# Kernel optimization log

Measured on AMD Instinct MI355X. Metric: run time of the kernel, lower is better.

Reference implementation:

```python
import jax, jax.numpy as jnp
import numpy as np

EPS = 1e-5


def instance_norm(x):
    # InstanceNorm2d(affine=False): normalize each (b, c) map over spatial dims
    mean = x.mean(axis=(2, 3), keepdims=True)
    var = ((x - mean) ** 2).mean(axis=(2, 3), keepdims=True)
    return (x - mean) / jnp.sqrt(var + EPS)


def adder_conv_transpose(x, w, stride, padding):
    """AdderNet transposed 'convolution': standard transposed-conv geometry
    (zero-dilate input by stride, pad by k-1-padding, slide flipped kernel),
    but with the multiply-accumulate replaced by negative L1 distance:
        out[b,co,h,w] = -sum_{ci,i,j} |x_patch[b,ci,h+i,w+j] - w_flip[co,ci,i,j]|
    x: (B, Cin, H, W); w: (Cin, Cout, k, k) as in nn.ConvTranspose2d.
    """
    Cin, Cout, k, _ = w.shape
    B, _, H, W = x.shape
    s = stride
    Hd, Wd = (H - 1) * s + 1, (W - 1) * s + 1
    xd = jnp.zeros((B, Cin, Hd, Wd), x.dtype).at[:, :, ::s, ::s].set(x)
    p = k - 1 - padding
    xp = jnp.pad(xd, ((0, 0), (0, 0), (p, p), (p, p)))
    wf = jnp.flip(w, axis=(2, 3)).transpose(1, 0, 2, 3)  # (Cout, Cin, k, k)
    Ho = Hd + 2 * p - k + 1
    Wo = Wd + 2 * p - k + 1
    out = jnp.zeros((B, Cout, Ho, Wo), x.dtype)
    # fixed k*k taps (<=16): accumulate -|patch - weight| summed over Cin
    for i in range(k):
        for j in range(k):
            patch = xp[:, :, i:i + Ho, j:j + Wo]  # (B, Cin, Ho, Wo)
            wij = wf[:, :, i, j][None, :, :, None, None]  # (1, Cout, Cin, 1, 1)
            out = out - jnp.abs(patch[:, None] - wij).sum(axis=2)
    return out


_CFG = [  # (Cin, Cout, k, stride, pad)
    (100, 128, 4, 2, 1),
    (128, 64, 4, 2, 1),
    (64, 32, 3, 2, 1),
    (32, 16, 4, 2, 1),
    (16, 1, 4, 2, 1),
]


def setup_inputs() -> dict:
    key = jax.random.key(0)
    ks = jax.random.split(key, 6)
    inp = {"x": jax.random.normal(ks[0], (512, 100, 1, 1), dtype=jnp.float32)}
    for li, (cin, cout, k, _, _) in enumerate(_CFG):
        inp[f"w{li + 1}"] = 0.1 * jax.random.normal(ks[li + 1], (cin, cout, k, k), dtype=jnp.float32)
    return inp


def reference(x, w1, w2, w3, w4, w5):
    h = x
    for w, (_, _, k, s, p) in zip((w1, w2, w3, w4, w5), _CFG):
        h = adder_conv_transpose(h, w, s, p)
        h = instance_norm(h)
        h = jax.nn.relu(h)
    # final activation is Tanh (last ReLU in loop replaced below)
    return jnp.tanh(instance_norm(adder_conv_transpose_final_fixup(h)))


# NOTE: structure above would double-apply the last layer; define reference cleanly instead.

def adder_conv_transpose_final_fixup(h):  # placeholder, unused
    return h


def reference(x, w1, w2, w3, w4, w5):  # noqa: F811 (clean final definition)
    ws = (w1, w2, w3, w4, w5)
    h = x
    for li, (w, (_, _, k, s, p)) in enumerate(zip(ws, _CFG)):
        h = instance_norm(adder_conv_transpose(h, w, s, p))
        h = jnp.tanh(h) if li == 4 else jax.nn.relu(h)
    return h  # (B, 1, 28, 28)
```

## Files before the change

### kernel.cpp

```cpp
#include <hip/hip_runtime.h>
#include <math.h>


#define OFF_T1 0
#define OFF_T2 2048
#define OFF_T3 3072
#define OFF_T4 3360
#define OFF_T5 3616
#define OFF_S  3632
#define OFF_WT1 4096
#define OFF_WT2 208896
#define OFF_WT3 339968
#define OFF_WT4 358400
#define OFF_WT5 366592
#define OFF_BUF0 366848
#define OFF_BUF1 1169664

__global__ __launch_bounds__(256) void prep1(const float* __restrict__ w1, const float* __restrict__ w2,
                      const float* __restrict__ w3, const float* __restrict__ w4,
                      const float* __restrict__ w5, float* __restrict__ ws) {
  int idx = blockIdx.x * 256 + threadIdx.x;
  if (idx < 362752) {
    const float* W; int CIN, COUT, KK, e, wtb;
    if (idx < 204800)      { W=w1; CIN=100; COUT=128; KK=16; e=idx;        wtb=OFF_WT1; }
    else if (idx < 335872) { W=w2; CIN=128; COUT=64;  KK=16; e=idx-204800; wtb=OFF_WT2; }
    else if (idx < 354304) { W=w3; CIN=64;  COUT=32;  KK=9;  e=idx-335872; wtb=OFF_WT3; }
    else if (idx < 362496) { W=w4; CIN=32;  COUT=16;  KK=16; e=idx-354304; wtb=OFF_WT4; }
    else                   { W=w5; CIN=16;  COUT=1;   KK=16; e=idx-362496; wtb=OFF_WT5; }
    int ci = e / (COUT*KK); int rem = e % (COUT*KK); int co = rem / KK; int r = rem % KK;
    ws[wtb + ((r*(CIN/4) + (ci>>2))*COUT + co)*4 + (ci&3)] = W[e];
  }
  if (idx < 3632) {
    const float* W; int CIN, COUT, KK, local;
    if (idx < 2048)      { W=w1; CIN=100; COUT=128; KK=16; local=idx; }
    else if (idx < 3072) { W=w2; CIN=128; COUT=64;  KK=16; local=idx-2048; }
    else if (idx < 3360) { W=w3; CIN=64;  COUT=32;  KK=9;  local=idx-3072; }
    else if (idx < 3616) { W=w4; CIN=32;  COUT=16;  KK=16; local=idx-3360; }
    else                 { W=w5; CIN=16;  COUT=1;   KK=16; local=idx-3616; }
    int co = local / KK, r = local % KK;
    float s = 0.f;
    for (int ci = 0; ci < CIN; ++ci) s += fabsf(W[(ci*COUT + co)*KK + r]);
    ws[idx] = s;
  }
}

__global__ __launch_bounds__(256) void prep2(float* __restrict__ ws) {
  int idx = threadIdx.x;
  if (idx >= 241) return;
  int tb, KK;
  if (idx < 128)      { tb = OFF_T1 + idx*16;       KK=16; }
  else if (idx < 192) { tb = OFF_T2 + (idx-128)*16; KK=16; }
  else if (idx < 224) { tb = OFF_T3 + (idx-192)*9;  KK=9;  }
  else if (idx < 240) { tb = OFF_T4 + (idx-224)*16; KK=16; }
  else                { tb = OFF_T5;                KK=16; }
  float s = 0.f;
  for (int r = 0; r < KK; ++r) s += ws[tb + r];
  ws[OFF_S + idx] = s;
}

template<int CIN, int COUT, int K, int STRIDE, int PAD,
         int HI, int WI, int HO, int WO, int ACT, int CP>
__global__ __launch_bounds__(256)
void layer_kernel(const float* __restrict__ X, const float* __restrict__ WT,
                  const float* __restrict__ T, const float* __restrict__ SS,
                  float* __restrict__ Y) {
  constexpr int S = HO*WO;
  constexpr int HIWI = HI*WI;
  constexpr int NIN = CIN*HIWI;
  constexpr int CIN4 = CIN/4;
  __shared__ float xst[HIWI*CIN];
  __shared__ float outs[S*CP];
  __shared__ float stat_mean[COUT], stat_rstd[COUT];
  __shared__ float wred[8];
  const int b = blockIdx.x;
  const int tid = threadIdx.x;

  for (int i = tid; i < NIN; i += 256) {
    int ci = i / HIWI, p = i % HIWI;
    xst[p*CIN + ci] = X[b*NIN + i];
  }
  __syncthreads();

  for (int idx = tid; idx < COUT*S; idx += 256) {
    const int co = idx % COUT;
    const int s  = idx / COUT;
    const int oh = s / WO, ow = s % WO;
    float acc = SS[co];
    #pragma unroll
    for (int kh = 0; kh < K; ++kh) {
      const int th = oh + PAD - kh;
      if (th < 0) continue;
      if (th % STRIDE) continue;
      const int ih = th / STRIDE;
      if (ih >= HI) continue;
      #pragma unroll
      for (int kw = 0; kw < K; ++kw) {
        const int tw = ow + PAD - kw;
        if (tw < 0) continue;
        if (tw % STRIDE) continue;
        const int iw = tw / STRIDE;
        if (iw >= WI) continue;
        const int r = kh*K + kw;
        acc -= T[co*(K*K) + r];
        const float4* xp4 = reinterpret_cast<const float4*>(&xst[(ih*WI + iw)*CIN]);
        const float4* wp4 = reinterpret_cast<const float4*>(WT) + (size_t)r*CIN4*COUT + co;
        float a0=0.f, a1=0.f, a2=0.f, a3=0.f;
        #pragma unroll 2
        for (int c4 = 0; c4 < CIN4; ++c4) {
          float4 xv = xp4[c4];
          float4 wv = wp4[(size_t)c4*COUT];
          a0 += fabsf(xv.x - wv.x);
          a1 += fabsf(xv.y - wv.y);
          a2 += fabsf(xv.z - wv.z);
          a3 += fabsf(xv.w - wv.w);
        }
        acc += (a0+a1) + (a2+a3);
      }
    }
    outs[s*CP + co] = -acc;
  }
  __syncthreads();

  if constexpr (COUT == 1) {
    float p = 0.f;
    for (int s2 = tid; s2 < S; s2 += 256) p += outs[s2];
    #pragma unroll
    for (int off = 1; off < 64; off <<= 1) p += __shfl_xor(p, off, 64);
    if ((tid & 63) == 0) wred[tid >> 6] = p;
    __syncthreads();
    const float mean = (wred[0]+wred[1]+wred[2]+wred[3]) * (1.f/S);
    float q = 0.f;
    for (int s2 = tid; s2 < S; s2 += 256) { float d = outs[s2]-mean; q += d*d; }
    #pragma unroll
    for (int off = 1; off < 64; off <<= 1) q += __shfl_xor(q, off, 64);
    __syncthreads();
    if ((tid & 63) == 0) wred[tid >> 6] = q;
    __syncthreads();
    const float rstd = rsqrtf((wred[0]+wred[1]+wred[2]+wred[3]) * (1.f/S) + 1e-5f);
    if (tid == 0) { stat_mean[0] = mean; stat_rstd[0] = rstd; }
    __syncthreads();
  } else {
    constexpr int G = 256 / COUT;
    const int g = tid / G;
    const int j = tid % G;
    float p = 0.f;
    for (int s2 = j; s2 < S; s2 += G) p += outs[s2*CP + g];
    #pragma unroll
    for (int off = 1; off < G; off <<= 1) p += __shfl_xor(p, off, 64);
    const float mean = p * (1.f/S);
    float q = 0.f;
    for (int s2 = j; s2 < S; s2 += G) { float d = outs[s2*CP + g] - mean; q += d*d; }
    #pragma unroll
    for (int off = 1; off < G; off <<= 1) q += __shfl_xor(q, off, 64);
    const float rstd = rsqrtf(q * (1.f/S) + 1e-5f);
    if (j == 0) { stat_mean[g] = mean; stat_rstd[g] = rstd; }
    __syncthreads();
  }

  for (int idx = tid; idx < COUT*S; idx += 256) {
    const int co = idx / S;
    const int s2 = idx % S;
    float v = (outs[s2*CP + co] - stat_mean[co]) * stat_rstd[co];
    v = ACT ? tanhf(v) : fmaxf(v, 0.f);
    Y[(size_t)b*(COUT*S) + idx] = v;
  }
}

extern "C" void kernel_launch(void* const* d_in, const int* in_sizes, int n_in,
                              void* d_out, int out_size, void* d_ws, size_t ws_size,
                              hipStream_t stream) {
  const float* x  = (const float*)d_in[0];
  const float* w1 = (const float*)d_in[1];
  const float* w2 = (const float*)d_in[2];
  const float* w3 = (const float*)d_in[3];
  const float* w4 = (const float*)d_in[4];
  const float* w5 = (const float*)d_in[5];
  float* ws  = (float*)d_ws;
  float* out = (float*)d_out;

  prep1<<<1417, 256, 0, stream>>>(w1, w2, w3, w4, w5, ws);
  prep2<<<1, 256, 0, stream>>>(ws);

  float* A1 = ws + OFF_BUF0;
  float* A2 = ws + OFF_BUF1;
  float* A3 = ws + OFF_BUF0;
  float* A4 = ws + OFF_BUF1;

  layer_kernel<100, 128, 4, 2, 1,  1, 1,  2, 2,  0, 129><<<512,256,0,stream>>>(x,  ws+OFF_WT1, ws+OFF_T1, ws+OFF_S,       A1);
  layer_kernel<128,  64, 4, 2, 1,  2, 2,  4, 4,  0,  65><<<512,256,0,stream>>>(A1, ws+OFF_WT2, ws+OFF_T2, ws+OFF_S+128,   A2);
  layer_kernel< 64,  32, 3, 2, 1,  4, 4,  7, 7,  0,  33><<<512,256,0,stream>>>(A2, ws+OFF_WT3, ws+OFF_T3, ws+OFF_S+192,   A3);
  layer_kernel< 32,  16, 4, 2, 1,  7, 7, 14,14,  0,  17><<<512,256,0,stream>>>(A3, ws+OFF_WT4, ws+OFF_T4, ws+OFF_S+224,   A4);
  layer_kernel< 16,   1, 4, 2, 1, 14,14, 28,28,  1,   1><<<512,256,0,stream>>>(A4, ws+OFF_WT5, ws+OFF_T5, ws+OFF_S+240,   out);
}
```

Before: 304.5 us.

## Restructure layers into batch-parallel conv kernels plus separate norm kernels

Replaces the per-sample fused layer kernel with a conv kernel that puts the batch on lanes (activations stored channel-major with batch innermost), register-tiles over output channels and batch, and splits the Cin reduction across blocks for some layers. Instance norm, ReLU and tanh move into separate norm kernels that also sum the Cin partial results. Padding taps are folded in through precomputed per-tap weight abs sums. The aim is better weight reuse across the batch and more parallelism, at the cost of extra launches and global round trips for the intermediate results.

Result: faster. 253.8 us (-16.7%).

```diff
diff --git a/kernel.cpp b/kernel.cpp
--- a/kernel.cpp
+++ b/kernel.cpp
@@ -1,24 +1,33 @@
 #include <hip/hip_runtime.h>
 #include <math.h>
 
+#define NB 512
 
 #define OFF_T1 0
 #define OFF_T2 2048
 #define OFF_T3 3072
 #define OFF_T4 3360
 #define OFF_T5 3616
-#define OFF_S  3632
 #define OFF_WT1 4096
 #define OFF_WT2 208896
 #define OFF_WT3 339968
 #define OFF_WT4 358400
 #define OFF_WT5 366592
-#define OFF_BUF0 366848
-#define OFF_BUF1 1169664
-
-__global__ __launch_bounds__(256) void prep1(const float* __restrict__ w1, const float* __restrict__ w2,
-                      const float* __restrict__ w3, const float* __restrict__ w4,
-                      const float* __restrict__ w5, float* __restrict__ ws) {
+#define OFF_ACT 366848
+#define OFF_Y   1972480
+
+__device__ __forceinline__ void loadv(float (&d)[1], const float* p){ d[0]=*p; }
+__device__ __forceinline__ void loadv(float (&d)[2], const float* p){ float2 v=*reinterpret_cast<const float2*>(p); d[0]=v.x; d[1]=v.y; }
+__device__ __forceinline__ void loadv(float (&d)[4], const float* p){ float4 v=*reinterpret_cast<const float4*>(p); d[0]=v.x; d[1]=v.y; d[2]=v.z; d[3]=v.w; }
+__device__ __forceinline__ void storev(float* p, const float (&d)[1]){ *p=d[0]; }
+__device__ __forceinline__ void storev(float* p, const float (&d)[2]){ *reinterpret_cast<float2*>(p)=make_float2(d[0],d[1]); }
+__device__ __forceinline__ void storev(float* p, const float (&d)[4]){ *reinterpret_cast<float4*>(p)=make_float4(d[0],d[1],d[2],d[3]); }
+
+__global__ __launch_bounds__(256)
+void prep1(const float* __restrict__ w1, const float* __restrict__ w2,
+           const float* __restrict__ w3, const float* __restrict__ w4,
+           const float* __restrict__ w5, const float* __restrict__ x,
+           float* __restrict__ ws) {
   int idx = blockIdx.x * 256 + threadIdx.x;
   if (idx < 362752) {
     const float* W; int CIN, COUT, KK, e, wtb;
@@ -28,141 +37,185 @@
     else if (idx < 362496) { W=w4; CIN=32;  COUT=16;  KK=16; e=idx-354304; wtb=OFF_WT4; }
     else                   { W=w5; CIN=16;  COUT=1;   KK=16; e=idx-362496; wtb=OFF_WT5; }
     int ci = e / (COUT*KK); int rem = e % (COUT*KK); int co = rem / KK; int r = rem % KK;
-    ws[wtb + ((r*(CIN/4) + (ci>>2))*COUT + co)*4 + (ci&3)] = W[e];
-  }
-  if (idx < 3632) {
-    const float* W; int CIN, COUT, KK, local;
-    if (idx < 2048)      { W=w1; CIN=100; COUT=128; KK=16; local=idx; }
-    else if (idx < 3072) { W=w2; CIN=128; COUT=64;  KK=16; local=idx-2048; }
-    else if (idx < 3360) { W=w3; CIN=64;  COUT=32;  KK=9;  local=idx-3072; }
-    else if (idx < 3616) { W=w4; CIN=32;  COUT=16;  KK=16; local=idx-3360; }
-    else                 { W=w5; CIN=16;  COUT=1;   KK=16; local=idx-3616; }
-    int co = local / KK, r = local % KK;
-    float s = 0.f;
-    for (int ci = 0; ci < CIN; ++ci) s += fabsf(W[(ci*COUT + co)*KK + r]);
-    ws[idx] = s;
-  }
-}
-
-__global__ __launch_bounds__(256) void prep2(float* __restrict__ ws) {
-  int idx = threadIdx.x;
-  if (idx >= 241) return;
-  int tb, KK;
-  if (idx < 128)      { tb = OFF_T1 + idx*16;       KK=16; }
-  else if (idx < 192) { tb = OFF_T2 + (idx-128)*16; KK=16; }
-  else if (idx < 224) { tb = OFF_T3 + (idx-192)*9;  KK=9;  }
-  else if (idx < 240) { tb = OFF_T4 + (idx-224)*16; KK=16; }
-  else                { tb = OFF_T5;                KK=16; }
+    ws[wtb + (r*CIN + ci)*COUT + co] = W[e];
+  } else {
+    int j = idx - 362752;
+    int b = j / 100, ci = j % 100;
+    ws[OFF_ACT + ci*NB + b] = x[j];
+  }
+}
+
+__global__ __launch_bounds__(256)
+void prep2(float* __restrict__ ws) {
+  int t = blockIdx.x * 256 + threadIdx.x;
+  if (t >= 3632) return;
+  int CIN, COUT, wtb, tb, local;
+  if (t < 2048)      { CIN=100; COUT=128; wtb=OFF_WT1; tb=OFF_T1; local=t; }
+  else if (t < 3072) { CIN=128; COUT=64;  wtb=OFF_WT2; tb=OFF_T2; local=t-2048; }
+  else if (t < 3360) { CIN=64;  COUT=32;  wtb=OFF_WT3; tb=OFF_T3; local=t-3072; }
+  else if (t < 3616) { CIN=32;  COUT=16;  wtb=OFF_WT4; tb=OFF_T4; local=t-3360; }
+  else               { CIN=16;  COUT=1;   wtb=OFF_WT5; tb=OFF_T5; local=t-3616; }
+  int r = local / COUT, co = local % COUT;
+  const float* wp = ws + wtb + (r*CIN)*COUT + co;
   float s = 0.f;
-  for (int r = 0; r < KK; ++r) s += ws[tb + r];
-  ws[OFF_S + idx] = s;
-}
-
-template<int CIN, int COUT, int K, int STRIDE, int PAD,
-         int HI, int WI, int HO, int WO, int ACT, int CP>
-__global__ __launch_bounds__(256)
-void layer_kernel(const float* __restrict__ X, const float* __restrict__ WT,
-                  const float* __restrict__ T, const float* __restrict__ SS,
-                  float* __restrict__ Y) {
-  constexpr int S = HO*WO;
-  constexpr int HIWI = HI*WI;
-  constexpr int NIN = CIN*HIWI;
-  constexpr int CIN4 = CIN/4;
-  __shared__ float xst[HIWI*CIN];
-  __shared__ float outs[S*CP];
-  __shared__ float stat_mean[COUT], stat_rstd[COUT];
-  __shared__ float wred[8];
-  const int b = blockIdx.x;
-  const int tid = threadIdx.x;
-
-  for (int i = tid; i < NIN; i += 256) {
-    int ci = i / HIWI, p = i % HIWI;
-    xst[p*CIN + ci] = X[b*NIN + i];
-  }
-  __syncthreads();
-
-  for (int idx = tid; idx < COUT*S; idx += 256) {
-    const int co = idx % COUT;
-    const int s  = idx / COUT;
-    const int oh = s / WO, ow = s % WO;
-    float acc = SS[co];
+  for (int ci = 0; ci < CIN; ++ci) s += fabsf(wp[ci*COUT]);
+  ws[tb + local] = s;
+}
+
+template<int CIN,int COUT,int K,int PAD,int HI,int WI,int HO,int WO,int R_CO,int R_B,int CS>
+__global__ __launch_bounds__(64)
+void conv_kernel(const float* __restrict__ X, const float* __restrict__ W,
+                 const float* __restrict__ T, float* __restrict__ Y) {
+  constexpr int S = HO*WO, NCOG = COUT/R_CO, NBG = NB/(64*R_B), CINS = CIN/CS;
+  const int wid = blockIdx.x;
+  const int q   = wid % S;
+  const int t1  = wid / S;
+  const int cog = t1 % NCOG;
+  const int t2  = t1 / NCOG;
+  const int bg  = t2 % NBG;
+  const int cs  = t2 / NBG;
+  const int oh = q / WO, ow = q % WO;
+  const int co0 = cog * R_CO;
+  const int b0  = bg*(64*R_B) + (int)threadIdx.x * R_B;
+  const int ci0 = cs * CINS;
+
+  float acc[R_CO][R_B];
+  #pragma unroll
+  for (int rc = 0; rc < R_CO; ++rc)
+    #pragma unroll
+    for (int rb = 0; rb < R_B; ++rb) acc[rc][rb] = 0.f;
+
+  if (cs == 0) {
+    float init[R_CO];
+    #pragma unroll
+    for (int rc = 0; rc < R_CO; ++rc) init[rc] = 0.f;
     #pragma unroll
     for (int kh = 0; kh < K; ++kh) {
-      const int th = oh + PAD - kh;
-      if (th < 0) continue;
-      if (th % STRIDE) continue;
-      const int ih = th / STRIDE;
-      if (ih >= HI) continue;
       #pragma unroll
       for (int kw = 0; kw < K; ++kw) {
-        const int tw = ow + PAD - kw;
-        if (tw < 0) continue;
-        if (tw % STRIDE) continue;
-        const int iw = tw / STRIDE;
-        if (iw >= WI) continue;
-        const int r = kh*K + kw;
-        acc -= T[co*(K*K) + r];
-        const float4* xp4 = reinterpret_cast<const float4*>(&xst[(ih*WI + iw)*CIN]);
-        const float4* wp4 = reinterpret_cast<const float4*>(WT) + (size_t)r*CIN4*COUT + co;
-        float a0=0.f, a1=0.f, a2=0.f, a3=0.f;
-        #pragma unroll 2
-        for (int c4 = 0; c4 < CIN4; ++c4) {
-          float4 xv = xp4[c4];
-          float4 wv = wp4[(size_t)c4*COUT];
-          a0 += fabsf(xv.x - wv.x);
-          a1 += fabsf(xv.y - wv.y);
-          a2 += fabsf(xv.z - wv.z);
-          a3 += fabsf(xv.w - wv.w);
+        const int th = oh + PAD - kh, tw = ow + PAD - kw;
+        const bool real = (th >= 0) && !(th & 1) && ((th >> 1) < HI)
+                       && (tw >= 0) && !(tw & 1) && ((tw >> 1) < WI);
+        if (!real) {
+          const float* tp = T + (kh*K + kw)*COUT + co0;
+          #pragma unroll
+          for (int rc = 0; rc < R_CO; ++rc) init[rc] += tp[rc];
         }
-        acc += (a0+a1) + (a2+a3);
       }
     }
-    outs[s*CP + co] = -acc;
-  }
-  __syncthreads();
-
-  if constexpr (COUT == 1) {
-    float p = 0.f;
-    for (int s2 = tid; s2 < S; s2 += 256) p += outs[s2];
-    #pragma unroll
-    for (int off = 1; off < 64; off <<= 1) p += __shfl_xor(p, off, 64);
-    if ((tid & 63) == 0) wred[tid >> 6] = p;
-    __syncthreads();
-    const float mean = (wred[0]+wred[1]+wred[2]+wred[3]) * (1.f/S);
-    float q = 0.f;
-    for (int s2 = tid; s2 < S; s2 += 256) { float d = outs[s2]-mean; q += d*d; }
-    #pragma unroll
-    for (int off = 1; off < 64; off <<= 1) q += __shfl_xor(q, off, 64);
-    __syncthreads();
-    if ((tid & 63) == 0) wred[tid >> 6] = q;
-    __syncthreads();
-    const float rstd = rsqrtf((wred[0]+wred[1]+wred[2]+wred[3]) * (1.f/S) + 1e-5f);
-    if (tid == 0) { stat_mean[0] = mean; stat_rstd[0] = rstd; }
-    __syncthreads();
-  } else {
-    constexpr int G = 256 / COUT;
-    const int g = tid / G;
-    const int j = tid % G;
-    float p = 0.f;
-    for (int s2 = j; s2 < S; s2 += G) p += outs[s2*CP + g];
-    #pragma unroll
-    for (int off = 1; off < G; off <<= 1) p += __shfl_xor(p, off, 64);
-    const float mean = p * (1.f/S);
-    float q = 0.f;
-    for (int s2 = j; s2 < S; s2 += G) { float d = outs[s2*CP + g] - mean; q += d*d; }
-    #pragma unroll
-    for (int off = 1; off < G; off <<= 1) q += __shfl_xor(q, off, 64);
-    const float rstd = rsqrtf(q * (1.f/S) + 1e-5f);
-    if (j == 0) { stat_mean[g] = mean; stat_rstd[g] = rstd; }
-    __syncthreads();
-  }
-
-  for (int idx = tid; idx < COUT*S; idx += 256) {
-    const int co = idx / S;
-    const int s2 = idx % S;
-    float v = (outs[s2*CP + co] - stat_mean[co]) * stat_rstd[co];
-    v = ACT ? tanhf(v) : fmaxf(v, 0.f);
-    Y[(size_t)b*(COUT*S) + idx] = v;
+    #pragma unroll
+    for (int rc = 0; rc < R_CO; ++rc)
+      #pragma unroll
+      for (int rb = 0; rb < R_B; ++rb) acc[rc][rb] = init[rc];
+  }
+
+  #pragma unroll
+  for (int kh = 0; kh < K; ++kh) {
+    const int th = oh + PAD - kh;
+    if (th < 0 || (th & 1)) continue;
+    const int ih = th >> 1;
+    if (ih >= HI) continue;
+    #pragma unroll
+    for (int kw = 0; kw < K; ++kw) {
+      const int tw = ow + PAD - kw;
+      if (tw < 0 || (tw & 1)) continue;
+      const int iw = tw >> 1;
+      if (iw >= WI) continue;
+      const int r = kh*K + kw, p = ih*WI + iw;
+      const float* xp = X + (p*CIN + ci0)*NB + b0;
+      const float* wp = W + (r*CIN + ci0)*COUT + co0;
+      #pragma unroll 4
+      for (int ci = 0; ci < CINS; ++ci) {
+        float xv[R_B];
+        loadv(xv, xp + ci*NB);
+        #pragma unroll
+        for (int rc = 0; rc < R_CO; ++rc) {
+          const float wv = wp[ci*COUT + rc];
+          #pragma unroll
+          for (int rb = 0; rb < R_B; ++rb)
+            acc[rc][rb] += fabsf(xv[rb] - wv);
+        }
+      }
+    }
+  }
+
+  float* yp = Y + ((cs*S + q)*COUT + co0)*NB + b0;
+  #pragma unroll
+  for (int rc = 0; rc < R_CO; ++rc) storev(yp + rc*NB, acc[rc]);
+}
+
+template<int COUT,int S,int CS>
+__global__ __launch_bounds__(256)
+void norm_kernel(const float* __restrict__ Y, float* __restrict__ A) {
+  __shared__ float red[4][64];
+  __shared__ float stat[2][64];
+  const int co = blockIdx.x % COUT;
+  const int bg = blockIdx.x / COUT;
+  const int lane = threadIdx.x & 63;
+  const int w = threadIdx.x >> 6;
+  const int b = bg*64 + lane;
+  const float* yb = Y + co*NB + b;
+
+  float s = 0.f;
+  for (int q = w; q < S; q += 4) {
+    float v = 0.f;
+    #pragma unroll
+    for (int cs = 0; cs < CS; ++cs) v += yb[(cs*S + q)*COUT*NB];
+    s += v;
+  }
+  red[w][lane] = s;
+  __syncthreads();
+  if (w == 0) stat[0][lane] = (red[0][lane]+red[1][lane]+red[2][lane]+red[3][lane]) * (1.f/S);
+  __syncthreads();
+  const float mu = stat[0][lane];
+
+  float s2 = 0.f;
+  for (int q = w; q < S; q += 4) {
+    float v = 0.f;
+    #pragma unroll
+    for (int cs = 0; cs < CS; ++cs) v += yb[(cs*S + q)*COUT*NB];
+    const float d = v - mu;
+    s2 += d*d;
+  }
+  red[w][lane] = s2;
+  __syncthreads();
+  if (w == 0) stat[1][lane] = rsqrtf((red[0][lane]+red[1][lane]+red[2][lane]+red[3][lane]) * (1.f/S) + 1e-5f);
+  __syncthreads();
+  const float rs = stat[1][lane];
+
+  for (int q = w; q < S; q += 4) {
+    float v = 0.f;
+    #pragma unroll
+    for (int cs = 0; cs < CS; ++cs) v += yb[(cs*S + q)*COUT*NB];
+    const float n = (mu - v) * rs;
+    A[(q*COUT + co)*NB + b] = fmaxf(n, 0.f);
+  }
+}
+
+__global__ __launch_bounds__(256)
+void norm5_kernel(const float* __restrict__ Y, float* __restrict__ out) {
+  const int w = threadIdx.x >> 6, lane = threadIdx.x & 63;
+  const int b = blockIdx.x*4 + w;
+  const float* yb = Y + b;
+
+  float s = 0.f;
+  for (int q = lane; q < 784; q += 64) s += yb[q*NB];
+  #pragma unroll
+  for (int off = 1; off < 64; off <<= 1) s += __shfl_xor(s, off, 64);
+  const float mu = s * (1.f/784.f);
+
+  float s2 = 0.f;
+  for (int q = lane; q < 784; q += 64) { float d = yb[q*NB] - mu; s2 += d*d; }
+  #pragma unroll
+  for (int off = 1; off < 64; off <<= 1) s2 += __shfl_xor(s2, off, 64);
+  const float rs = rsqrtf(s2*(1.f/784.f) + 1e-5f);
+
+  for (int q = lane; q < 784; q += 64) {
+    const float n = (mu - yb[q*NB]) * rs;
+    const float ax = fabsf(n);
+    const float e = __expf(-2.f*ax);
+    const float t = (1.f - e) / (1.f + e);
+    out[b*784 + q] = copysignf(t, n);
   }
 }
 
@@ -178,17 +231,24 @@
   float* ws  = (float*)d_ws;
   float* out = (float*)d_out;
 
-  prep1<<<1417, 256, 0, stream>>>(w1, w2, w3, w4, w5, ws);
-  prep2<<<1, 256, 0, stream>>>(ws);
-
-  float* A1 = ws + OFF_BUF0;
-  float* A2 = ws + OFF_BUF1;
-  float* A3 = ws + OFF_BUF0;
-  float* A4 = ws + OFF_BUF1;
-
-  layer_kernel<100, 128, 4, 2, 1,  1, 1,  2, 2,  0, 129><<<512,256,0,stream>>>(x,  ws+OFF_WT1, ws+OFF_T1, ws+OFF_S,       A1);
-  layer_kernel<128,  64, 4, 2, 1,  2, 2,  4, 4,  0,  65><<<512,256,0,stream>>>(A1, ws+OFF_WT2, ws+OFF_T2, ws+OFF_S+128,   A2);
-  layer_kernel< 64,  32, 3, 2, 1,  4, 4,  7, 7,  0,  33><<<512,256,0,stream>>>(A2, ws+OFF_WT3, ws+OFF_T3, ws+OFF_S+192,   A3);
-  layer_kernel< 32,  16, 4, 2, 1,  7, 7, 14,14,  0,  17><<<512,256,0,stream>>>(A3, ws+OFF_WT4, ws+OFF_T4, ws+OFF_S+224,   A4);
-  layer_kernel< 16,   1, 4, 2, 1, 14,14, 28,28,  1,   1><<<512,256,0,stream>>>(A4, ws+OFF_WT5, ws+OFF_T5, ws+OFF_S+240,   out);
-}
+  float* ACT = ws + OFF_ACT;
+  float* Y   = ws + OFF_Y;
+
+  prep1<<<1617, 256, 0, stream>>>(w1, w2, w3, w4, w5, x, ws);
+  prep2<<<15, 256, 0, stream>>>(ws);
+
+  conv_kernel<100,128,4,1,  1, 1,  2, 2, 4,2,1><<< 512,64,0,stream>>>(ACT, ws+OFF_WT1, ws+OFF_T1, Y);
+  norm_kernel<128,  4,1><<<1024,256,0,stream>>>(Y, ACT);
+
+  conv_kernel<128, 64,4,1,  2, 2,  4, 4, 4,2,2><<<2048,64,0,stream>>>(ACT, ws+OFF_WT2, ws+OFF_T2, Y);
+  norm_kernel< 64, 16,2><<< 512,256,0,stream>>>(Y, ACT);
+
+  conv_kernel< 64, 32,3,1,  4, 4,  7, 7, 4,2,2><<<3136,64,0,stream>>>(ACT, ws+OFF_WT3, ws+OFF_T3, Y);
+  norm_kernel< 32, 49,2><<< 256,256,0,stream>>>(Y, ACT);
+
+  conv_kernel< 32, 16,4,1,  7, 7, 14,14, 4,2,1><<<3136,64,0,stream>>>(ACT, ws+OFF_WT4, ws+OFF_T4, Y);
+  norm_kernel< 16,196,1><<< 128,256,0,stream>>>(Y, ACT);
+
+  conv_kernel< 16,  1,4,1, 14,14, 28,28, 1,4,1><<<1568,64,0,stream>>>(ACT, ws+OFF_WT5, ws+OFF_T5, Y);
+  norm5_kernel<<<128,256,0,stream>>>(Y, out);
+}
```

## Fuse all five adder-deconv layers into one persistent kernel with LDS ping-pong

Applied to the files above, without the earlier changes.

Replaces the five per-layer kernels and the two prep kernels with one prep kernel and a single fused kernel. Each 512-thread block processes two batch samples through all five layers, keeping activations in two LDS buffers and storing them in a channel-interleaved float4 layout. Outputs are computed per 2x2 stride-parity tile with branch-free masked taps, and the normalisation sign flip, ReLU and a fast tanh are folded into the norm stage. This removes inter-layer global round trips and launch overhead. In exchange it runs only 256 blocks at one block per CU and does redundant masked tap work at borders.

After: 320.2 us. 1.05x slower.

```diff
diff --git a/kernel.cpp b/kernel.cpp
--- a/kernel.cpp
+++ b/kernel.cpp
@@ -1,24 +1,26 @@
 #include <hip/hip_runtime.h>
 #include <math.h>
-
 
 #define OFF_T1 0
 #define OFF_T2 2048
 #define OFF_T3 3072
 #define OFF_T4 3360
 #define OFF_T5 3616
-#define OFF_S  3632
+#define OFF_S1 3632
+#define OFF_S2 3760
+#define OFF_S3 3824
+#define OFF_S4 3856
+#define OFF_S5 3872
 #define OFF_WT1 4096
 #define OFF_WT2 208896
 #define OFF_WT3 339968
 #define OFF_WT4 358400
 #define OFF_WT5 366592
-#define OFF_BUF0 366848
-#define OFF_BUF1 1169664
-
-__global__ __launch_bounds__(256) void prep1(const float* __restrict__ w1, const float* __restrict__ w2,
-                      const float* __restrict__ w3, const float* __restrict__ w4,
-                      const float* __restrict__ w5, float* __restrict__ ws) {
+
+__global__ __launch_bounds__(256)
+void prep(const float* __restrict__ w1, const float* __restrict__ w2,
+          const float* __restrict__ w3, const float* __restrict__ w4,
+          const float* __restrict__ w5, float* __restrict__ ws) {
   int idx = blockIdx.x * 256 + threadIdx.x;
   if (idx < 362752) {
     const float* W; int CIN, COUT, KK, e, wtb;
@@ -29,141 +31,191 @@
     else                   { W=w5; CIN=16;  COUT=1;   KK=16; e=idx-362496; wtb=OFF_WT5; }
     int ci = e / (COUT*KK); int rem = e % (COUT*KK); int co = rem / KK; int r = rem % KK;
     ws[wtb + ((r*(CIN/4) + (ci>>2))*COUT + co)*4 + (ci&3)] = W[e];
-  }
-  if (idx < 3632) {
-    const float* W; int CIN, COUT, KK, local;
-    if (idx < 2048)      { W=w1; CIN=100; COUT=128; KK=16; local=idx; }
-    else if (idx < 3072) { W=w2; CIN=128; COUT=64;  KK=16; local=idx-2048; }
-    else if (idx < 3360) { W=w3; CIN=64;  COUT=32;  KK=9;  local=idx-3072; }
-    else if (idx < 3616) { W=w4; CIN=32;  COUT=16;  KK=16; local=idx-3360; }
-    else                 { W=w5; CIN=16;  COUT=1;   KK=16; local=idx-3616; }
-    int co = local / KK, r = local % KK;
+  } else if (idx < 366384) {
+    int t = idx - 362752;
+    const float* W; int CIN, COUT, KK, tb, local;
+    if (t < 2048)      { W=w1; CIN=100; COUT=128; KK=16; tb=OFF_T1; local=t; }
+    else if (t < 3072) { W=w2; CIN=128; COUT=64;  KK=16; tb=OFF_T2; local=t-2048; }
+    else if (t < 3360) { W=w3; CIN=64;  COUT=32;  KK=9;  tb=OFF_T3; local=t-3072; }
+    else if (t < 3616) { W=w4; CIN=32;  COUT=16;  KK=16; tb=OFF_T4; local=t-3360; }
+    else               { W=w5; CIN=16;  COUT=1;   KK=16; tb=OFF_T5; local=t-3616; }
+    int r = local / COUT, co = local % COUT;
     float s = 0.f;
+    #pragma unroll 4
     for (int ci = 0; ci < CIN; ++ci) s += fabsf(W[(ci*COUT + co)*KK + r]);
-    ws[idx] = s;
-  }
-}
-
-__global__ __launch_bounds__(256) void prep2(float* __restrict__ ws) {
-  int idx = threadIdx.x;
-  if (idx >= 241) return;
-  int tb, KK;
-  if (idx < 128)      { tb = OFF_T1 + idx*16;       KK=16; }
-  else if (idx < 192) { tb = OFF_T2 + (idx-128)*16; KK=16; }
-  else if (idx < 224) { tb = OFF_T3 + (idx-192)*9;  KK=9;  }
-  else if (idx < 240) { tb = OFF_T4 + (idx-224)*16; KK=16; }
-  else                { tb = OFF_T5;                KK=16; }
-  float s = 0.f;
-  for (int r = 0; r < KK; ++r) s += ws[tb + r];
-  ws[OFF_S + idx] = s;
-}
-
-template<int CIN, int COUT, int K, int STRIDE, int PAD,
-         int HI, int WI, int HO, int WO, int ACT, int CP>
-__global__ __launch_bounds__(256)
-void layer_kernel(const float* __restrict__ X, const float* __restrict__ WT,
-                  const float* __restrict__ T, const float* __restrict__ SS,
-                  float* __restrict__ Y) {
-  constexpr int S = HO*WO;
-  constexpr int HIWI = HI*WI;
-  constexpr int NIN = CIN*HIWI;
-  constexpr int CIN4 = CIN/4;
-  __shared__ float xst[HIWI*CIN];
-  __shared__ float outs[S*CP];
-  __shared__ float stat_mean[COUT], stat_rstd[COUT];
-  __shared__ float wred[8];
-  const int b = blockIdx.x;
-  const int tid = threadIdx.x;
-
-  for (int i = tid; i < NIN; i += 256) {
-    int ci = i / HIWI, p = i % HIWI;
-    xst[p*CIN + ci] = X[b*NIN + i];
-  }
-  __syncthreads();
-
-  for (int idx = tid; idx < COUT*S; idx += 256) {
-    const int co = idx % COUT;
-    const int s  = idx / COUT;
-    const int oh = s / WO, ow = s % WO;
-    float acc = SS[co];
+    ws[tb + local] = s;
+  } else if (idx < 366625) {
+    int t = idx - 366384;
+    const float* W; int CIN, COUT, KK, sb, co;
+    if (t < 128)       { W=w1; CIN=100; COUT=128; KK=16; sb=OFF_S1; co=t; }
+    else if (t < 192)  { W=w2; CIN=128; COUT=64;  KK=16; sb=OFF_S2; co=t-128; }
+    else if (t < 224)  { W=w3; CIN=64;  COUT=32;  KK=9;  sb=OFF_S3; co=t-192; }
+    else if (t < 240)  { W=w4; CIN=32;  COUT=16;  KK=16; sb=OFF_S4; co=t-224; }
+    else               { W=w5; CIN=16;  COUT=1;   KK=16; sb=OFF_S5; co=t-240; }
+    float s = 0.f;
+    for (int ci = 0; ci < CIN; ++ci) {
+      const float* wp = W + (ci*COUT + co)*KK;
+      #pragma unroll 4
+      for (int r = 0; r < KK; ++r) s += fabsf(wp[r]);
+    }
+    ws[sb + co] = s;
+  }
+}
+
+template<int CIN,int COUT,int K,int HI,int WI,int HO,int WO,int T_L,int CO_LANE,int B_L>
+__device__ __forceinline__ void conv(const float* __restrict__ X, float* __restrict__ Y,
+                                     const float* __restrict__ WT, const float* __restrict__ Tt,
+                                     const float* __restrict__ Ss,
+                                     int wave, int lane) {
+  constexpr int CIN4 = CIN/4, S = HO*WO, THT = (HO+1)/2, TWT = (WO+1)/2;
+  constexpr int NTILES = THT*TWT;
+  constexpr int NTG = (NTILES + T_L - 1)/T_L, NCOG = COUT/CO_LANE, NBT = 2/B_L;
+  constexpr int NT = NTG*NCOG*NBT;
+  const int tl = lane / (CO_LANE*B_L);
+  const int lc = (lane / B_L) % CO_LANE;
+  const int lb = lane % B_L;
+  for (int t = wave; t < NT; t += 8) {
+    const int tg  = t % NTG;
+    const int r1  = t / NTG;
+    const int cog = r1 % NCOG;
+    const int tb  = r1 / NCOG;
+    const int b   = (B_L == 2) ? lb : tb;
+    const int co  = cog*CO_LANE + lc;
+    const int tile = tg*T_L + tl;
+    const bool tval = (tile < NTILES);
+    const int tc  = tval ? tile : 0;
+    const int th_ = tc / TWT, tw_ = tc % TWT;
+
+    const float base = Ss[co];
+    float acc[4] = {base, base, base, base};
     #pragma unroll
     for (int kh = 0; kh < K; ++kh) {
-      const int th = oh + PAD - kh;
-      if (th < 0) continue;
-      if (th % STRIDE) continue;
-      const int ih = th / STRIDE;
-      if (ih >= HI) continue;
+      const int dh = (kh+1)&1;
+      const int c1 = (dh + 1 - kh) >> 1;
+      const int ih = th_ + c1, oh = 2*th_ + dh;
+      const bool vh = (ih >= 0) && (ih < HI) && (oh < HO);
+      const int ihc = min(max(ih, 0), HI-1);
       #pragma unroll
       for (int kw = 0; kw < K; ++kw) {
-        const int tw = ow + PAD - kw;
-        if (tw < 0) continue;
-        if (tw % STRIDE) continue;
-        const int iw = tw / STRIDE;
-        if (iw >= WI) continue;
+        const int dw = (kw+1)&1;
+        const int c2 = (dw + 1 - kw) >> 1;
+        const int iw = tw_ + c2, ow = 2*tw_ + dw;
+        const bool vw = (iw >= 0) && (iw < WI) && (ow < WO);
+        const int iwc = min(max(iw, 0), WI-1);
+        const float maskf = (vh && vw && tval) ? 1.f : 0.f;
         const int r = kh*K + kw;
-        acc -= T[co*(K*K) + r];
-        const float4* xp4 = reinterpret_cast<const float4*>(&xst[(ih*WI + iw)*CIN]);
-        const float4* wp4 = reinterpret_cast<const float4*>(WT) + (size_t)r*CIN4*COUT + co;
-        float a0=0.f, a1=0.f, a2=0.f, a3=0.f;
-        #pragma unroll 2
-        for (int c4 = 0; c4 < CIN4; ++c4) {
-          float4 xv = xp4[c4];
-          float4 wv = wp4[(size_t)c4*COUT];
-          a0 += fabsf(xv.x - wv.x);
-          a1 += fabsf(xv.y - wv.y);
-          a2 += fabsf(xv.z - wv.z);
-          a3 += fabsf(xv.w - wv.w);
+        const float Tv = Tt[r*COUT + co];
+        const int pb = (ihc*WI + iwc)*2 + b;
+        const float4* xp = reinterpret_cast<const float4*>(X) + pb;
+        const float4* wp = reinterpret_cast<const float4*>(WT) + (size_t)r*CIN4*COUT + co;
+        float tap = 0.f;
+        #pragma unroll 4
+        for (int c = 0; c < CIN4; ++c) {
+          const float4 xv = xp[c*(2*HI*WI)];
+          const float4 wv = wp[c*COUT];
+          tap += fabsf(xv.x - wv.x) + fabsf(xv.y - wv.y)
+               + fabsf(xv.z - wv.z) + fabsf(xv.w - wv.w);
         }
-        acc += (a0+a1) + (a2+a3);
+        acc[dh*2+dw] += maskf*(tap - Tv);
       }
     }
-    outs[s*CP + co] = -acc;
-  }
-  __syncthreads();
-
-  if constexpr (COUT == 1) {
-    float p = 0.f;
-    for (int s2 = tid; s2 < S; s2 += 256) p += outs[s2];
     #pragma unroll
-    for (int off = 1; off < 64; off <<= 1) p += __shfl_xor(p, off, 64);
-    if ((tid & 63) == 0) wred[tid >> 6] = p;
-    __syncthreads();
-    const float mean = (wred[0]+wred[1]+wred[2]+wred[3]) * (1.f/S);
-    float q = 0.f;
-    for (int s2 = tid; s2 < S; s2 += 256) { float d = outs[s2]-mean; q += d*d; }
-    #pragma unroll
-    for (int off = 1; off < 64; off <<= 1) q += __shfl_xor(q, off, 64);
-    __syncthreads();
-    if ((tid & 63) == 0) wred[tid >> 6] = q;
-    __syncthreads();
-    const float rstd = rsqrtf((wred[0]+wred[1]+wred[2]+wred[3]) * (1.f/S) + 1e-5f);
-    if (tid == 0) { stat_mean[0] = mean; stat_rstd[0] = rstd; }
-    __syncthreads();
-  } else {
-    constexpr int G = 256 / COUT;
-    const int g = tid / G;
-    const int j = tid % G;
-    float p = 0.f;
-    for (int s2 = j; s2 < S; s2 += G) p += outs[s2*CP + g];
-    #pragma unroll
-    for (int off = 1; off < G; off <<= 1) p += __shfl_xor(p, off, 64);
-    const float mean = p * (1.f/S);
-    float q = 0.f;
-    for (int s2 = j; s2 < S; s2 += G) { float d = outs[s2*CP + g] - mean; q += d*d; }
-    #pragma unroll
-    for (int off = 1; off < G; off <<= 1) q += __shfl_xor(q, off, 64);
-    const float rstd = rsqrtf(q * (1.f/S) + 1e-5f);
-    if (j == 0) { stat_mean[g] = mean; stat_rstd[g] = rstd; }
-    __syncthreads();
-  }
-
-  for (int idx = tid; idx < COUT*S; idx += 256) {
-    const int co = idx / S;
-    const int s2 = idx % S;
-    float v = (outs[s2*CP + co] - stat_mean[co]) * stat_rstd[co];
-    v = ACT ? tanhf(v) : fmaxf(v, 0.f);
-    Y[(size_t)b*(COUT*S) + idx] = v;
-  }
+    for (int dh = 0; dh < 2; ++dh) {
+      #pragma unroll
+      for (int dw = 0; dw < 2; ++dw) {
+        const int oh = 2*th_ + dh, ow = 2*tw_ + dw;
+        if (tval && oh < HO && ow < WO)
+          Y[(co*2 + b)*S + oh*WO + ow] = acc[dh*2+dw];
+      }
+    }
+  }
+}
+
+template<int COUT,int S>
+__device__ __forceinline__ void norm(const float* __restrict__ Y, float* __restrict__ Xn, int tid) {
+  constexpr int NCH = COUT*2, PT = 512/NCH;
+  const int ch = tid / PT, j = tid % PT;
+  const int co = ch >> 1, b = ch & 1;
+  const float* yp = Y + ch*S;
+  float s = 0.f;
+  for (int q = j; q < S; q += PT) s += yp[q];
+  #pragma unroll
+  for (int off = 1; off < PT; off <<= 1) s += __shfl_xor(s, off, 64);
+  const float mu = s * (1.f/S);
+  float v = 0.f;
+  for (int q = j; q < S; q += PT) { const float d = yp[q] - mu; v += d*d; }
+  #pragma unroll
+  for (int off = 1; off < PT; off <<= 1) v += __shfl_xor(v, off, 64);
+  const float rs = rsqrtf(v * (1.f/S) + 1e-5f);
+  for (int q = j; q < S; q += PT) {
+    float n = (mu - yp[q]) * rs;
+    n = fmaxf(n, 0.f);
+    Xn[(((co>>2)*S + q)*2 + b)*4 + (co&3)] = n;
+  }
+}
+
+__device__ __forceinline__ void norm5(const float* __restrict__ Y, float* __restrict__ out,
+                                      int tid, int blk, float* __restrict__ scratch) {
+  const int b = tid >> 8, j = tid & 255;
+  const int wid = tid >> 6, lane = tid & 63;
+  const float* yp = Y + b*784;
+  float s = 0.f;
+  for (int q = j; q < 784; q += 256) s += yp[q];
+  #pragma unroll
+  for (int off = 1; off < 64; off <<= 1) s += __shfl_xor(s, off, 64);
+  if (lane == 0) scratch[wid] = s;
+  __syncthreads();
+  const float mu = (scratch[b*4] + scratch[b*4+1] + scratch[b*4+2] + scratch[b*4+3]) * (1.f/784.f);
+  __syncthreads();
+  float v = 0.f;
+  for (int q = j; q < 784; q += 256) { const float d = yp[q] - mu; v += d*d; }
+  #pragma unroll
+  for (int off = 1; off < 64; off <<= 1) v += __shfl_xor(v, off, 64);
+  if (lane == 0) scratch[wid] = v;
+  __syncthreads();
+  const float rs = rsqrtf((scratch[b*4] + scratch[b*4+1] + scratch[b*4+2] + scratch[b*4+3]) * (1.f/784.f) + 1e-5f);
+  for (int q = j; q < 784; q += 256) {
+    const float n = (mu - yp[q]) * rs;
+    const float ax = fabsf(n);
+    const float e = __expf(-2.f*ax);
+    out[(2*blk + b)*784 + q] = copysignf((1.f - e)/(1.f + e), n);
+  }
+}
+
+__global__ __launch_bounds__(512, 1)
+void fused_main(const float* __restrict__ x, const float* __restrict__ ws,
+                float* __restrict__ out) {
+  __shared__ float P[6272];
+  __shared__ float Q[6272];
+  __shared__ float scratch[8];
+  const int tid = threadIdx.x;
+  const int wave = tid >> 6, lane = tid & 63;
+  const int blk = blockIdx.x;
+
+  for (int t = tid; t < 200; t += 512) {
+    const int b = t / 100, ci = t % 100;
+    P[((ci>>2)*2 + b)*4 + (ci&3)] = x[(2*blk + b)*100 + ci];
+  }
+  __syncthreads();
+  conv<100,128,4, 1, 1, 2, 2,   1, 32, 2>(P, Q, ws+OFF_WT1, ws+OFF_T1, ws+OFF_S1, wave, lane);
+  __syncthreads();
+  norm<128, 4>(Q, P, tid);
+  __syncthreads();
+  conv<128, 64,4, 2, 2, 4, 4,   4, 16, 1>(P, Q, ws+OFF_WT2, ws+OFF_T2, ws+OFF_S2, wave, lane);
+  __syncthreads();
+  norm<64, 16>(Q, P, tid);
+  __syncthreads();
+  conv< 64, 32,3, 4, 4, 7, 7,  16,  4, 1>(P, Q, ws+OFF_WT3, ws+OFF_T3, ws+OFF_S3, wave, lane);
+  __syncthreads();
+  norm<32, 49>(Q, P, tid);
+  __syncthreads();
+  conv< 32, 16,4, 7, 7,14,14,  16,  4, 1>(P, Q, ws+OFF_WT4, ws+OFF_T4, ws+OFF_S4, wave, lane);
+  __syncthreads();
+  norm<16, 196>(Q, P, tid);
+  __syncthreads();
+  conv< 16,  1,4,14,14,28,28,  32,  1, 2>(P, Q, ws+OFF_WT5, ws+OFF_T5, ws+OFF_S5, wave, lane);
+  __syncthreads();
+  norm5(Q, out, tid, blk, scratch);
 }
 
 extern "C" void kernel_launch(void* const* d_in, const int* in_sizes, int n_in,
@@ -178,17 +230,6 @@
   float* ws  = (float*)d_ws;
   float* out = (float*)d_out;
 
-  prep1<<<1417, 256, 0, stream>>>(w1, w2, w3, w4, w5, ws);
-  prep2<<<1, 256, 0, stream>>>(ws);
-
-  float* A1 = ws + OFF_BUF0;
-  float* A2 = ws + OFF_BUF1;
-  float* A3 = ws + OFF_BUF0;
-  float* A4 = ws + OFF_BUF1;
-
-  layer_kernel<100, 128, 4, 2, 1,  1, 1,  2, 2,  0, 129><<<512,256,0,stream>>>(x,  ws+OFF_WT1, ws+OFF_T1, ws+OFF_S,       A1);
-  layer_kernel<128,  64, 4, 2, 1,  2, 2,  4, 4,  0,  65><<<512,256,0,stream>>>(A1, ws+OFF_WT2, ws+OFF_T2, ws+OFF_S+128,   A2);
-  layer_kernel< 64,  32, 3, 2, 1,  4, 4,  7, 7,  0,  33><<<512,256,0,stream>>>(A2, ws+OFF_WT3, ws+OFF_T3, ws+OFF_S+192,   A3);
-  layer_kernel< 32,  16, 4, 2, 1,  7, 7, 14,14,  0,  17><<<512,256,0,stream>>>(A3, ws+OFF_WT4, ws+OFF_T4, ws+OFF_S+224,   A4);
-  layer_kernel< 16,   1, 4, 2, 1, 14,14, 28,28,  1,   1><<<512,256,0,stream>>>(A4, ws+OFF_WT5, ws+OFF_T5, ws+OFF_S+240,   out);
-}
+  prep<<<1433, 256, 0, stream>>>(w1, w2, w3, w4, w5, ws);
+  fused_main<<<256, 512, 0, stream>>>(x, ws, out);
+}
```
